# Kernel optimization log

Hardware: AMD Instinct MI355X
Metric: run time of the kernel (lower is better)

The kernel has to match this reference:

```python
import jax, jax.numpy as jnp
import numpy as np

N_LAYERS = 4
D_MODEL = 768
EXPAND = 2
D_INNER = EXPAND * D_MODEL  # 1536
D_STATE = 16
D_CONV = 4
DT_RANK = (D_MODEL + 15) // 16  # 48
BATCH = 2
SEQLEN = 1024


def setup_inputs() -> dict:
    key = jax.random.key(0)
    ks = jax.random.split(key, 7)
    s = 0.02
    x = jax.random.normal(ks[0], (BATCH, SEQLEN, D_MODEL), jnp.float32)
    in_proj_w = jax.random.normal(ks[1], (N_LAYERS, 2 * D_INNER, D_MODEL), jnp.float32) * s
    conv_w = jax.random.normal(ks[2], (N_LAYERS, D_INNER, D_CONV), jnp.float32) * 0.1
    conv_b = jnp.zeros((N_LAYERS, D_INNER), jnp.float32)
    x_proj_w = jax.random.normal(ks[3], (N_LAYERS, DT_RANK + 2 * D_STATE, D_INNER), jnp.float32) * s
    dt_proj_w = jax.random.normal(ks[4], (N_LAYERS, D_INNER, DT_RANK), jnp.float32) * s
    dt_proj_b = jnp.full((N_LAYERS, D_INNER), -4.6, jnp.float32)  # softplus(-4.6) ~= 0.01
    A_log = jnp.broadcast_to(
        jnp.log(jnp.arange(1, D_STATE + 1, dtype=jnp.float32)), (N_LAYERS, D_INNER, D_STATE)
    ) + jnp.zeros((N_LAYERS, D_INNER, D_STATE), jnp.float32)
    D_param = jnp.ones((N_LAYERS, D_INNER), jnp.float32)
    out_proj_w = jax.random.normal(ks[5], (N_LAYERS, D_MODEL, D_INNER), jnp.float32) * s
    return {
        'x': x, 'in_proj_w': in_proj_w, 'conv_w': conv_w, 'conv_b': conv_b,
        'x_proj_w': x_proj_w, 'dt_proj_w': dt_proj_w, 'dt_proj_b': dt_proj_b,
        'A_log': A_log, 'D_param': D_param, 'out_proj_w': out_proj_w,
    }


def _mamba_block(x, ipw, cw, cb, xpw, dpw, dpb, alog, dparam, opw):
    Bsz = x.shape[0]
    # input projection -> gate z and ssm stream u
    xz = jnp.einsum('bld,ed->ble', x, ipw)          # [B,L,2*d_inner]
    u, z = jnp.split(xz, 2, axis=-1)
    # causal depthwise conv over time + silu
    uc = jnp.swapaxes(u, 1, 2)                      # [B,d_inner,L]
    uc = jax.lax.conv_general_dilated(
        uc, cw[:, None, :], (1,), [(D_CONV - 1, 0)],
        feature_group_count=D_INNER, dimension_numbers=('NCH', 'OIH', 'NCH'))
    u = jax.nn.silu(jnp.swapaxes(uc, 1, 2) + cb)    # [B,L,d_inner]
    # input-dependent SSM parameters
    x_dbl = jnp.einsum('bld,ed->ble', u, xpw)       # [B,L,dt_rank+2*d_state]
    dt, Bm, C = jnp.split(x_dbl, [DT_RANK, DT_RANK + D_STATE], axis=-1)
    delta = jax.nn.softplus(jnp.einsum('blr,dr->bld', dt, dpw) + dpb)  # [B,L,d_inner]
    A = -jnp.exp(alog)                              # [d_inner,d_state]
    dA = jnp.exp(delta[..., None] * A)              # [B,L,d_inner,d_state]
    dBu = (delta * u)[..., None] * Bm[:, :, None, :]  # [B,L,d_inner,d_state]

    def step(h, inp):
        dA_t, dBu_t, C_t = inp
        h = dA_t * h + dBu_t                        # [B,d_inner,d_state]
        return h, jnp.einsum('bdn,bn->bd', h, C_t)

    h0 = jnp.zeros((Bsz, D_INNER, D_STATE), x.dtype)
    _, ys = jax.lax.scan(
        step, h0,
        (jnp.swapaxes(dA, 0, 1), jnp.swapaxes(dBu, 0, 1), jnp.swapaxes(C, 0, 1)))
    y = jnp.swapaxes(ys, 0, 1) + u * dparam         # [B,L,d_inner]
    y = y * jax.nn.silu(z)
    return jnp.einsum('bld,ed->ble', y, opw)        # [B,L,d_model]


def reference(x, in_proj_w, conv_w, conv_b, x_proj_w, dt_proj_w, dt_proj_b, A_log, D_param, out_proj_w):
    for i in range(N_LAYERS):
        x = _mamba_block(x, in_proj_w[i], conv_w[i], conv_b[i], x_proj_w[i],
                         dt_proj_w[i], dt_proj_b[i], A_log[i], D_param[i], out_proj_w[i])
    return x
```

## Files before the change

kernel.cpp:

```cpp
#include <hip/hip_runtime.h>
#include <math.h>

#define NL 4
#define DMODEL 768
#define DINNER 1536
#define DSTATE 16
#define DCONV 4
#define DTRANK 48
#define BATCH 2
#define SEQLEN 1024
#define MTOK (BATCH*SEQLEN)
#define XDIM 80
#define KPAD 64
#define NPAD 96
#define KS2 16
#define KS4 4
#define NCHUNK 64
#define NCSHIFT 6
#define CLEN 16
#define CHSTRIDE (BATCH*16*DINNER)

typedef __bf16 bf16x8 __attribute__((ext_vector_type(8)));
typedef float f32x4 __attribute__((ext_vector_type(4)));

__device__ __forceinline__ void splitbf(float f, unsigned short& hi, unsigned short& lo) {
    unsigned uh = __float_as_uint(f);
    unsigned rh = uh + (0x7fffu + ((uh >> 16) & 1u));
    unsigned short h = (unsigned short)(rh >> 16);
    float fh = __uint_as_float(((unsigned)h) << 16);
    float r = f - fh;
    unsigned ul = __float_as_uint(r);
    unsigned rl = ul + (0x7fffu + ((ul >> 16) & 1u));
    hi = h;
    lo = (unsigned short)(rl >> 16);
}

__device__ __forceinline__ void splitbf4(float4 v, ushort4& h, ushort4& l) {
    splitbf(v.x, h.x, l.x);
    splitbf(v.y, h.y, l.y);
    splitbf(v.z, h.z, l.z);
    splitbf(v.w, h.w, l.w);
}

__device__ __forceinline__ float bf2f(unsigned short h) {
    return __uint_as_float(((unsigned)h) << 16);
}

__device__ __forceinline__ unsigned short f2bf(float f) {
    unsigned u = __float_as_uint(f);
    unsigned r = u + (0x7fffu + ((u >> 16) & 1u));
    return (unsigned short)(r >> 16);
}

__device__ __forceinline__ void pow16(float p, float* pw) {
    float p2 = p * p, p4 = p2 * p2, p8 = p4 * p4;
    pw[0]  = p;          pw[1]  = p2;         pw[2]  = p2 * p;     pw[3]  = p4;
    pw[4]  = p4 * p;     pw[5]  = p4 * p2;    pw[6]  = p4 * pw[2]; pw[7]  = p8;
    pw[8]  = p8 * p;     pw[9]  = p8 * p2;    pw[10] = p8 * pw[2]; pw[11] = p8 * p4;
    pw[12] = p8 * pw[4]; pw[13] = p8 * pw[5]; pw[14] = p8 * pw[6]; pw[15] = p8 * p8;
}

__device__ __forceinline__ void gload_lds16(const void* g, void* l) {
    __builtin_amdgcn_global_load_lds(
        (const __attribute__((address_space(1))) unsigned*)g,
        (__attribute__((address_space(3))) unsigned*)l, 16, 0, 0);
}

#define N_IPW (2 * DINNER * DMODEL / 4)
#define N_OPW (DMODEL * DINNER / 4)
#define N_XPW (NPAD * DINNER / 4)
#define N_DPW (DINNER * KPAD / 4)
#define N_DTP (MTOK * (KPAD - DTRANK) / 4)
#define N_PREP (N_IPW + N_OPW + N_XPW + N_DPW + N_DTP)
#define N_XSPL (MTOK * DMODEL / 4)

__global__ __launch_bounds__(256) void prep_all(
    const float* __restrict__ ipw, const float* __restrict__ opw,
    const float* __restrict__ xpw, const float* __restrict__ dpw,
    const float* __restrict__ x,
    unsigned short* __restrict__ wih, unsigned short* __restrict__ wil,
    unsigned short* __restrict__ woh, unsigned short* __restrict__ wol,
    unsigned short* __restrict__ wxh,
    unsigned short* __restrict__ wdh,
    unsigned short* __restrict__ dth,
    unsigned short* __restrict__ ah, unsigned short* __restrict__ al)
{
    const int L = blockIdx.y;
    int i = blockIdx.x * 256 + threadIdx.x;
    if (i < N_IPW) {
        float4 v = ((const float4*)(ipw + (size_t)L * 2 * DINNER * DMODEL))[i];
        ushort4 h, l;
        splitbf4(v, h, l);
        size_t o = (size_t)L * N_IPW + i;
        ((ushort4*)wih)[o] = h;
        ((ushort4*)wil)[o] = l;
        return;
    }
    i -= N_IPW;
    if (i < N_OPW) {
        float4 v = ((const float4*)(opw + (size_t)L * DMODEL * DINNER))[i];
        ushort4 h, l;
        splitbf4(v, h, l);
        size_t o = (size_t)L * N_OPW + i;
        ((ushort4*)woh)[o] = h;
        ((ushort4*)wol)[o] = l;
        return;
    }
    i -= N_OPW;
    if (i < N_XPW) {
        int e = i * 4;
        int row = e / DINNER, col = e % DINNER;
        ushort4 h = {0, 0, 0, 0}, l = {0, 0, 0, 0};
        if (row < XDIM) {
            float4 v = *(const float4*)(xpw + (size_t)L * XDIM * DINNER + (size_t)row * DINNER + col);
            splitbf4(v, h, l);
        }
        size_t o = (size_t)L * N_XPW + i;
        ((ushort4*)wxh)[o] = h;
        return;
    }
    i -= N_XPW;
    if (i < N_DPW) {
        int e = i * 4;
        int row = e >> 6, col = e & 63;
        ushort4 h = {0, 0, 0, 0}, l = {0, 0, 0, 0};
        if (col < DTRANK) {
            float4 v = *(const float4*)(dpw + (size_t)L * DINNER * DTRANK + (size_t)row * DTRANK + col);
            splitbf4(v, h, l);
        }
        size_t o = (size_t)L * N_DPW + i;
        ((ushort4*)wdh)[o] = h;
        return;
    }
    i -= N_DPW;
    if (L != 0) return;
    if (i < N_DTP) {
        int e = i * 4;
        int row = e >> 4, col = DTRANK + (e & 15);
        int o = (row * KPAD + col) / 4;
        ushort4 z = {0, 0, 0, 0};
        ((ushort4*)dth)[o] = z;
        return;
    }
    i -= N_DTP;
    if (i < N_XSPL) {
        float4 v = ((const float4*)x)[i];
        ushort4 h, l;
        splitbf4(v, h, l);
        ((ushort4*)ah)[i] = h;
        ((ushort4*)al)[i] = l;
    }
}

template<int BM, int BN, int BK, int EPI, int PREC>
__global__ __launch_bounds__(256, (BM >= 128 ? 2 : 4)) void gemm_pre(
    const unsigned short* __restrict__ Ah, const unsigned short* __restrict__ Al, int lda,
    const unsigned short* __restrict__ Wh, const unsigned short* __restrict__ Wl, int ldw,
    float* __restrict__ C, float* __restrict__ Caux, int ldc, int Klen, size_t zstride, int nclip,
    const float* __restrict__ bias)
{
    constexpr int MT = BM / 32, NT = BN / 32;
    constexpr int WPR = BK / 8;
    constexpr int ACH = BM * WPR;
    constexpr int WCH = BN * WPR;
    __shared__ unsigned short sAh[BM * BK];
    __shared__ unsigned short sWh[BN * BK];
    __shared__ unsigned short sAl[PREC == 0 ? BM * BK : 8];
    __shared__ unsigned short sWl[PREC == 0 ? BN * BK : 8];

    const int tid = threadIdx.x;
    const int m0 = blockIdx.y * BM, n0 = blockIdx.x * BN;
    const int kbase = blockIdx.z * Klen;
    C += (size_t)blockIdx.z * zstride;
    const int lane = tid & 63, wave = tid >> 6;
    const int wr = wave >> 1, wc = wave & 1;
    const int wm0 = wr * (BM / 2), wn0 = wc * (BN / 2);
    const int lrow = lane & 15, lq = lane >> 4;

    const bool use_lo = (PREC == 0) && !(EPI == 1 && n0 >= DINNER);

    f32x4 acc[MT][NT];
    #pragma unroll
    for (int mt = 0; mt < MT; mt++)
        #pragma unroll
        for (int nt = 0; nt < NT; nt++) {
            f32x4 z = {0.f, 0.f, 0.f, 0.f};
            acc[mt][nt] = z;
        }

    for (int k0 = kbase; k0 < kbase + Klen; k0 += BK) {
        #pragma unroll
        for (int i = 0; i < (ACH + 255) / 256; i++) {
            int chunk = i * 256 + tid;
            if (ACH % 256 == 0 || chunk < ACH) {
                int r = chunk / WPR, cp = chunk % WPR;
                int c = (BK == 32) ? (cp ^ ((r >> 1) & 3)) : (cp ^ (r & 7));
                size_t goff = (size_t)(m0 + r) * lda + k0 + c * 8;
                gload_lds16(Ah + goff, &sAh[chunk * 8]);
                if (use_lo) gload_lds16(Al + goff, &sAl[chunk * 8]);
            }
        }
        #pragma unroll
        for (int i = 0; i < (WCH + 255) / 256; i++) {
            int chunk = i * 256 + tid;
            if (WCH % 256 == 0 || chunk < WCH) {
                int r = chunk / WPR, cp = chunk % WPR;
                int c = (BK == 32) ? (cp ^ ((r >> 1) & 3)) : (cp ^ (r & 7));
                size_t goff = (size_t)(n0 + r) * ldw + k0 + c * 8;
                gload_lds16(Wh + goff, &sWh[chunk * 8]);
                if (use_lo) gload_lds16(Wl + goff, &sWl[chunk * 8]);
            }
        }
        __syncthreads();

        #pragma unroll
        for (int kk = 0; kk < BK / 32; kk++) {
            bf16x8 fah[MT], fal[MT], fwh[NT], fwl[NT];
            #pragma unroll
            for (int mt = 0; mt < MT; mt++) {
                int rr = wm0 + mt * 16 + lrow;
                int w = (BK == 32) ? (lq ^ ((rr >> 1) & 3)) : ((kk * 4 + lq) ^ (rr & 7));
                int off = rr * BK + w * 8;
                fah[mt] = *(const bf16x8*)&sAh[off];
                if (use_lo) fal[mt] = *(const bf16x8*)&sAl[off];
            }
            #pragma unroll
            for (int nt = 0; nt < NT; nt++) {
                int rr = wn0 + nt * 16 + lrow;
                int w = (BK == 32) ? (lq ^ ((rr >> 1) & 3)) : ((kk * 4 + lq) ^ (rr & 7));
                int off = rr * BK + w * 8;
                fwh[nt] = *(const bf16x8*)&sWh[off];
                if (use_lo) fwl[nt] = *(const bf16x8*)&sWl[off];
            }
            #pragma unroll
            for (int mt = 0; mt < MT; mt++)
                #pragma unroll
                for (int nt = 0; nt < NT; nt++)
                    acc[mt][nt] = __builtin_amdgcn_mfma_f32_16x16x32_bf16(fah[mt], fwh[nt], acc[mt][nt], 0, 0, 0);
            if (use_lo) {
                #pragma unroll
                for (int mt = 0; mt < MT; mt++)
                    #pragma unroll
                    for (int nt = 0; nt < NT; nt++) {
                        acc[mt][nt] = __builtin_amdgcn_mfma_f32_16x16x32_bf16(fah[mt], fwl[nt], acc[mt][nt], 0, 0, 0);
                        acc[mt][nt] = __builtin_amdgcn_mfma_f32_16x16x32_bf16(fal[mt], fwh[nt], acc[mt][nt], 0, 0, 0);
                    }
            }
        }
        __syncthreads();
    }

    #pragma unroll
    for (int mt = 0; mt < MT; mt++)
        #pragma unroll
        for (int nt = 0; nt < NT; nt++) {
            int row0 = m0 + wm0 + mt * 16 + lq * 4;
            int col  = n0 + wn0 + nt * 16 + lrow;
            if constexpr (EPI == 0) {
                #pragma unroll
                for (int i = 0; i < 4; i++)
                    if (col < nclip) C[(size_t)(row0 + i) * ldc + col] = acc[mt][nt][i];
            } else if constexpr (EPI == 1) {
                if (col < DINNER) {
                    #pragma unroll
                    for (int i = 0; i < 4; i++)
                        C[(size_t)(row0 + i) * DINNER + col] = acc[mt][nt][i];
                } else {
                    #pragma unroll
                    for (int i = 0; i < 4; i++)
                        Caux[(size_t)(row0 + i) * DINNER + (col - DINNER)] = acc[mt][nt][i];
                }
            } else {
                unsigned short* Cb = (unsigned short*)C;
                float bc = bias[col];
                #pragma unroll
                for (int i = 0; i < 4; i++) {
                    float t = acc[mt][nt][i] + bc;
                    float e = __expf(-fabsf(t));
                    float v = fmaxf(t, 0.f) + __logf(1.f + e);
                    Cb[(size_t)(row0 + i) * ldc + col] = f2bf(v);
                }
            }
        }
}

template<int MODE>
__global__ __launch_bounds__(256) void reduce4(
    const float* __restrict__ part, float* __restrict__ dst,
    unsigned short* __restrict__ hi, unsigned short* __restrict__ lo)
{
    constexpr size_t S = (size_t)MTOK * DMODEL / 4;
    int i = blockIdx.x * 256 + threadIdx.x;
    const float4* p = (const float4*)part;
    float4 a = p[i], b = p[i + S], c = p[i + 2 * S], d = p[i + 3 * S];
    float4 s = {a.x + b.x + c.x + d.x, a.y + b.y + c.y + d.y,
                a.z + b.z + c.z + d.z, a.w + b.w + c.w + d.w};
    if (MODE == 0) {
        ((float4*)dst)[i] = s;
    } else {
        ushort4 h, l;
        splitbf4(s, h, l);
        ((ushort4*)hi)[i] = h;
        ((ushort4*)lo)[i] = l;
    }
}

__global__ __launch_bounds__(256) void reduce16(
    const float* __restrict__ part, float* __restrict__ xdbl,
    unsigned short* __restrict__ dth)
{
    constexpr int N4 = MTOK * XDIM / 4;
    constexpr int S4 = MTOK * XDIM / 4;
    int i = blockIdx.x * 256 + threadIdx.x;
    if (i >= N4) return;
    const float4* p = (const float4*)part;
    float4 s = {0.f, 0.f, 0.f, 0.f};
    #pragma unroll
    for (int z = 0; z < KS2; z++) {
        float4 v = p[(size_t)z * S4 + i];
        s.x += v.x; s.y += v.y; s.z += v.z; s.w += v.w;
    }
    ((float4*)xdbl)[i] = s;
    int e = i * 4;
    int col = e % XDIM, row = e / XDIM;
    if (col < DTRANK) {
        ushort4 h, l;
        splitbf4(s, h, l);
        int o = (row * KPAD + col) / 4;
        ((ushort4*)dth)[o] = h;
    }
}

__global__ __launch_bounds__(256) void conv_silu_kernel(
    const float* __restrict__ xu, const float* __restrict__ cw,
    const float* __restrict__ cb,
    unsigned short* __restrict__ uh, unsigned* __restrict__ ut)
{
    int idx = blockIdx.x * 256 + threadIdx.x;
    int d = idx % DINNER;
    int rblk = idx / DINNER;
    int b = rblk >> 6;
    int l0 = (rblk & 63) * 16;
    const float* base = xu + ((size_t)b * SEQLEN + l0) * DINNER + d;
    float w0 = cw[d * 4 + 0], w1 = cw[d * 4 + 1], w2 = cw[d * 4 + 2], w3 = cw[d * 4 + 3];
    float bias = cb[d];
    float xv[19];
    #pragma unroll
    for (int j = 0; j < 3; j++)
        xv[j] = (l0 + j >= 3) ? base[(j - 3) * DINNER] : 0.f;
    #pragma unroll
    for (int j = 3; j < 19; j++)
        xv[j] = base[(j - 3) * DINNER];
    #pragma unroll
    for (int i = 0; i < 16; i++) {
        float acc = bias;
        acc = fmaf(w0, xv[i], acc);
        acc = fmaf(w1, xv[i + 1], acc);
        acc = fmaf(w2, xv[i + 2], acc);
        acc = fmaf(w3, xv[i + 3], acc);
        float uv = acc / (1.f + __expf(-acc));
        unsigned short h, lo_;
        splitbf(uv, h, lo_);
        size_t o = ((size_t)b * SEQLEN + l0 + i) * DINNER + d;
        uh[o] = h;
        ut[o] = ((unsigned)h << 16) | (unsigned)lo_;
    }
}

__global__ __launch_bounds__(256, 3) void scan_pass1(
    const unsigned short* __restrict__ delta, const unsigned* __restrict__ ut,
    const float* __restrict__ xdbl,
    unsigned short* __restrict__ qbuf, float* __restrict__ sdlbuf)
{
    int gid = blockIdx.x * 256 + threadIdx.x;
    int d = gid % DINNER;
    int r = gid / DINNER;
    int chunk = r & (NCHUNK - 1);
    int b = r >> NCSHIFT;
    float q[16];
    #pragma unroll
    for (int n = 0; n < 16; n++) q[n] = 0.f;
    float sdl = 0.f;
    size_t rowbase = (size_t)b * SEQLEN * DINNER + d;
    int t0 = chunk * CLEN;
    #pragma unroll 4
    for (int i = 0; i < CLEN; i++) {
        int t = t0 + i;
        size_t o = rowbase + (size_t)t * DINNER;
        float dl = bf2f(delta[o]);
        unsigned upk = ut[o];
        float uu = bf2f((unsigned short)(upk >> 16)) + bf2f((unsigned short)(upk & 0xffffu));
        float du = dl * uu;
        sdl += dl;
        float pw[16];
        pow16(__expf(-dl), pw);
        const float* Bp = xdbl + (size_t)(b * SEQLEN + t) * XDIM + DTRANK;
        float Bf[16];
        *(float4*)&Bf[0]  = *(const float4*)(Bp + 0);
        *(float4*)&Bf[4]  = *(const float4*)(Bp + 4);
        *(float4*)&Bf[8]  = *(const float4*)(Bp + 8);
        *(float4*)&Bf[12] = *(const float4*)(Bp + 12);
        #pragma unroll
        for (int n = 0; n < 16; n++)
            q[n] = fmaf(pw[n], q[n], du * Bf[n]);
    }
    size_t off = (size_t)((chunk * BATCH + b) * 16) * DINNER + d;
    #pragma unroll
    for (int n = 0; n < 16; n++)
        qbuf[off + (size_t)n * DINNER] = f2bf(q[n]);
    sdlbuf[(size_t)(chunk * BATCH + b) * DINNER + d] = sdl;
}

__global__ __launch_bounds__(256) void scan_pass2(
    const unsigned short* __restrict__ qbuf, const float* __restrict__ sdlbuf,
    unsigned short* __restrict__ hinit)
{
    __shared__ float sP[8][32];
    __shared__ float sQ[8][32];
    int g = threadIdx.x & 31;
    int s = threadIdx.x >> 5;
    int t = blockIdx.x * 32 + g;
    int d = t % DINNER;
    int b = t / (16 * DINNER);
    int n = (t / DINNER) & 15;
    float Arow = -(float)(n + 1);
    float q[8], p[8];
    #pragma unroll
    for (int j = 0; j < 8; j++) {
        int c = s * 8 + j;
        q[j] = bf2f(qbuf[(size_t)c * CHSTRIDE + t]);
        float sdl = sdlbuf[(size_t)(c * BATCH + b) * DINNER + d];
        p[j] = __expf(Arow * sdl);
    }
    float h = 0.f, P = 1.f;
    #pragma unroll
    for (int j = 0; j < 8; j++) {
        h = fmaf(p[j], h, q[j]);
        P *= p[j];
    }
    sP[s][g] = P;
    sQ[s][g] = h;
    __syncthreads();
    float h0 = 0.f;
    for (int j = 0; j < s; j++)
        h0 = fmaf(sP[j][g], h0, sQ[j][g]);
    #pragma unroll
    for (int j = 0; j < 8; j++) {
        int c = s * 8 + j;
        hinit[(size_t)c * CHSTRIDE + t] = f2bf(h0);
        h0 = fmaf(p[j], h0, q[j]);
    }
}

__global__ __launch_bounds__(256, 3) void scan_pass3(
    const unsigned short* __restrict__ delta, const unsigned* __restrict__ ut,
    const float* __restrict__ xdbl, const float* __restrict__ zs,
    const float* __restrict__ Dp, const unsigned short* __restrict__ hinit,
    unsigned short* __restrict__ yh, unsigned short* __restrict__ yl)
{
    int gid = blockIdx.x * 256 + threadIdx.x;
    int d = gid % DINNER;
    int r = gid / DINNER;
    int chunk = r & (NCHUNK - 1);
    int b = r >> NCSHIFT;
    float h[16];
    size_t hoff = (size_t)chunk * CHSTRIDE + (size_t)(b * 16) * DINNER + d;
    #pragma unroll
    for (int n = 0; n < 16; n++) h[n] = bf2f(hinit[hoff + (size_t)n * DINNER]);
    float Dpar = Dp[d];
    size_t rowbase = (size_t)b * SEQLEN * DINNER + d;
    int t0 = chunk * CLEN;
    #pragma unroll 4
    for (int i = 0; i < CLEN; i++) {
        int t = t0 + i;
        size_t o = rowbase + (size_t)t * DINNER;
        float dl = bf2f(delta[o]);
        unsigned upk = ut[o];
        float uu = bf2f((unsigned short)(upk >> 16)) + bf2f((unsigned short)(upk & 0xffffu));
        float du = dl * uu;
        float pw[16];
        pow16(__expf(-dl), pw);
        const float* Bp = xdbl + (size_t)(b * SEQLEN + t) * XDIM + DTRANK;
        float Bf[16], Cf[16];
        *(float4*)&Bf[0]  = *(const float4*)(Bp + 0);
        *(float4*)&Bf[4]  = *(const float4*)(Bp + 4);
        *(float4*)&Bf[8]  = *(const float4*)(Bp + 8);
        *(float4*)&Bf[12] = *(const float4*)(Bp + 12);
        *(float4*)&Cf[0]  = *(const float4*)(Bp + 16);
        *(float4*)&Cf[4]  = *(const float4*)(Bp + 20);
        *(float4*)&Cf[8]  = *(const float4*)(Bp + 24);
        *(float4*)&Cf[12] = *(const float4*)(Bp + 28);
        float yt = 0.f;
        #pragma unroll
        for (int n = 0; n < 16; n++) {
            h[n] = fmaf(pw[n], h[n], du * Bf[n]);
            yt = fmaf(h[n], Cf[n], yt);
        }
        yt = fmaf(uu, Dpar, yt);
        float z = zs[o];
        float sz = z / (1.f + __expf(-z));
        float yv = yt * sz;
        unsigned short hh, ll;
        splitbf(yv, hh, ll);
        yh[o] = hh;
        yl[o] = ll;
    }
}

extern "C" void kernel_launch(void* const* d_in, const int* in_sizes, int n_in,
                              void* d_out, int out_size, void* d_ws, size_t ws_size,
                              hipStream_t stream) {
    const float* x    = (const float*)d_in[0];
    const float* ipw  = (const float*)d_in[1];
    const float* cw   = (const float*)d_in[2];
    const float* cb   = (const float*)d_in[3];
    const float* xpw  = (const float*)d_in[4];
    const float* dpw  = (const float*)d_in[5];
    const float* dpb  = (const float*)d_in[6];
    const float* alog = (const float*)d_in[7];
    const float* dpar = (const float*)d_in[8];
    const float* opw  = (const float*)d_in[9];
    float* out = (float*)d_out;
    (void)alog;

    char* ws = (char*)d_ws;
    float* xu     = (float*)ws;           ws += (size_t)MTOK * DINNER * 4;
    float* zs     = (float*)ws;           ws += (size_t)MTOK * DINNER * 4;
    unsigned short* delta = (unsigned short*)ws; ws += (size_t)MTOK * DINNER * 4;
    float* xdbl   = (float*)ws;           ws += (size_t)MTOK * XDIM * 4;
    unsigned short* qbuf  = (unsigned short*)ws; ws += (size_t)NCHUNK * CHSTRIDE * 4;
    unsigned short* hinit = (unsigned short*)ws; ws += (size_t)NCHUNK * CHSTRIDE * 4;
    float* sdlb   = (float*)ws;           ws += (size_t)NCHUNK * BATCH * DINNER * 4;
    float* part   = (float*)ws;           ws += (size_t)4 * MTOK * DMODEL * 4;
    unsigned short* ah  = (unsigned short*)ws; ws += (size_t)MTOK * DMODEL * 2;
    unsigned short* al  = (unsigned short*)ws; ws += (size_t)MTOK * DMODEL * 2;
    unsigned short* yh  = (unsigned short*)ws; ws += (size_t)MTOK * DINNER * 2;
    unsigned short* yl  = (unsigned short*)ws; ws += (size_t)MTOK * DINNER * 2;
    unsigned short* uh  = (unsigned short*)ws; ws += (size_t)MTOK * DINNER * 2;
    unsigned* ut        = (unsigned*)ws;       ws += (size_t)MTOK * DINNER * 4;
    unsigned short* wih = (unsigned short*)ws; ws += (size_t)NL * 2 * DINNER * DMODEL * 2;
    unsigned short* wil = (unsigned short*)ws; ws += (size_t)NL * 2 * DINNER * DMODEL * 2;
    unsigned short* woh = (unsigned short*)ws; ws += (size_t)NL * DMODEL * DINNER * 2;
    unsigned short* wol = (unsigned short*)ws; ws += (size_t)NL * DMODEL * DINNER * 2;
    unsigned short* wxh = (unsigned short*)ws; ws += (size_t)NL * NPAD * DINNER * 2;
    unsigned short* wdh = (unsigned short*)ws; ws += (size_t)NL * DINNER * KPAD * 2;
    unsigned short* dth = (unsigned short*)ws; ws += (size_t)MTOK * KPAD * 2;

    prep_all<<<dim3((N_PREP + N_XSPL) / 256, NL), 256, 0, stream>>>(
        ipw, opw, xpw, dpw, x,
        wih, wil, woh, wol, wxh, wdh, dth, ah, al);

    for (int L = 0; L < NL; L++) {
        const float* cw_l   = cw   + (size_t)L * DINNER * DCONV;
        const float* cb_l   = cb   + (size_t)L * DINNER;
        const float* dpb_l  = dpb  + (size_t)L * DINNER;
        const float* dpar_l = dpar + (size_t)L * DINNER;
        const unsigned short* wih_l = wih + (size_t)L * 2 * DINNER * DMODEL;
        const unsigned short* wil_l = wil + (size_t)L * 2 * DINNER * DMODEL;
        const unsigned short* woh_l = woh + (size_t)L * DMODEL * DINNER;
        const unsigned short* wol_l = wol + (size_t)L * DMODEL * DINNER;
        const unsigned short* wxh_l = wxh + (size_t)L * NPAD * DINNER;
        const unsigned short* wdh_l = wdh + (size_t)L * DINNER * KPAD;

        gemm_pre<128, 96, 64, 1, 0><<<dim3(2 * DINNER / 96, MTOK / 128, 1), 256, 0, stream>>>(
            ah, al, DMODEL, wih_l, wil_l, DMODEL, xu, zs, DINNER, DMODEL, 0, 1 << 30, nullptr);

        conv_silu_kernel<<<(MTOK / 16) * DINNER / 256, 256, 0, stream>>>(xu, cw_l, cb_l, uh, ut);

        gemm_pre<64, 96, 32, 0, 1><<<dim3(1, MTOK / 64, KS2), 256, 0, stream>>>(
            uh, nullptr, DINNER, wxh_l, nullptr, DINNER, part, nullptr, XDIM,
            DINNER / KS2, (size_t)MTOK * XDIM, XDIM, nullptr);
        reduce16<<<(MTOK * XDIM / 4 + 255) / 256, 256, 0, stream>>>(part, xdbl, dth);

        gemm_pre<128, 96, 64, 2, 1><<<dim3(DINNER / 96, MTOK / 128, 1), 256, 0, stream>>>(
            dth, nullptr, KPAD, wdh_l, nullptr, KPAD, (float*)delta, nullptr, DINNER, KPAD, 0, 1 << 30, dpb_l);

        scan_pass1<<<(BATCH * NCHUNK * DINNER) / 256, 256, 0, stream>>>(
            delta, ut, xdbl, qbuf, sdlb);
        scan_pass2<<<CHSTRIDE * 8 / 256, 256, 0, stream>>>(qbuf, sdlb, hinit);
        scan_pass3<<<(BATCH * NCHUNK * DINNER) / 256, 256, 0, stream>>>(
            delta, ut, xdbl, zs, dpar_l, hinit, yh, yl);

        gemm_pre<128, 96, 64, 0, 0><<<dim3(DMODEL / 96, MTOK / 128, KS4), 256, 0, stream>>>(
            yh, yl, DINNER, woh_l, wol_l, DINNER, part, nullptr, DMODEL,
            DINNER / KS4, (size_t)MTOK * DMODEL, 1 << 30, nullptr);

        int rblocks = MTOK * DMODEL / 4 / 256;
        if (L == NL - 1) {
            reduce4<0><<<rblocks, 256, 0, stream>>>(part, out, nullptr, nullptr);
        } else {
            reduce4<1><<<rblocks, 256, 0, stream>>>(part, nullptr, ah, al);
        }
    }
    (void)in_sizes; (void)n_in; (void)out_size; (void)ws_size;
}
```

Before: 567.4 us.

## Fuse causal conv and SiLU into the x_proj split-K GEMM prologue

Removes the standalone conv_silu kernel and computes the depthwise causal conv plus SiLU inside a new x_proj GEMM kernel. Each block builds its 64x96 bf16 u tile directly in shared memory and writes the packed hi/lo value to ut for the scan. This removes the uh buffer write and re-read along with one kernel launch per layer. The cost is that each block re-reads 4 time-shifted rows of xu, so there is some redundant global traffic, and the stores to ut are now scattered across many small blocks.

After: 641.7 us. 13.1% more time.

```diff
diff --git a/kernel.cpp b/kernel.cpp
--- a/kernel.cpp
+++ b/kernel.cpp
@@ -284,6 +284,99 @@
         }
 }
 
+__global__ __launch_bounds__(256, 4) void gemm2_conv(
+    const float* __restrict__ xu, const float* __restrict__ cw,
+    const float* __restrict__ cb, const unsigned short* __restrict__ Wh,
+    float* __restrict__ part, unsigned* __restrict__ ut)
+{
+    __shared__ unsigned short sU[64 * 112];
+    __shared__ unsigned short sWh[96 * 32];
+    const int tid = threadIdx.x;
+    const int m0 = blockIdx.y * 64;
+    const int kb = blockIdx.z * 96;
+    float* C = part + (size_t)blockIdx.z * ((size_t)MTOK * XDIM);
+
+    #pragma unroll
+    for (int i = 0; i < 24; i++) {
+        int idx = i * 256 + tid;
+        int r = idx / 96, c = idx % 96;
+        int t = m0 + r;
+        int l = t & (SEQLEN - 1);
+        int d = kb + c;
+        const float* bp = xu + (size_t)t * DINNER + d;
+        float w0 = cw[d * 4 + 0], w1 = cw[d * 4 + 1], w2 = cw[d * 4 + 2], w3 = cw[d * 4 + 3];
+        float acc = cb[d];
+        if (l >= 3) acc = fmaf(w0, bp[-3 * DINNER], acc);
+        if (l >= 2) acc = fmaf(w1, bp[-2 * DINNER], acc);
+        if (l >= 1) acc = fmaf(w2, bp[-1 * DINNER], acc);
+        acc = fmaf(w3, bp[0], acc);
+        float uv = acc / (1.f + __expf(-acc));
+        unsigned short h, lo_;
+        splitbf(uv, h, lo_);
+        sU[r * 112 + c] = h;
+        ut[(size_t)t * DINNER + d] = ((unsigned)h << 16) | (unsigned)lo_;
+    }
+
+    const int lane = tid & 63, wave = tid >> 6;
+    const int wr = wave >> 1, wc = wave & 1;
+    const int wm0 = wr * 32, wn0 = wc * 48;
+    const int lrow = lane & 15, lq = lane >> 4;
+
+    f32x4 acc[2][3];
+    #pragma unroll
+    for (int mt = 0; mt < 2; mt++)
+        #pragma unroll
+        for (int nt = 0; nt < 3; nt++) {
+            f32x4 z = {0.f, 0.f, 0.f, 0.f};
+            acc[mt][nt] = z;
+        }
+
+    #pragma unroll
+    for (int ks = 0; ks < 3; ks++) {
+        #pragma unroll
+        for (int i = 0; i < 2; i++) {
+            int chunk = i * 256 + tid;
+            if (chunk < 384) {
+                int r = chunk >> 2, cp = chunk & 3;
+                int c = cp ^ ((r >> 1) & 3);
+                size_t goff = (size_t)r * DINNER + kb + ks * 32 + c * 8;
+                gload_lds16(Wh + goff, &sWh[chunk * 8]);
+            }
+        }
+        __syncthreads();
+
+        bf16x8 fah[2], fwh[3];
+        #pragma unroll
+        for (int mt = 0; mt < 2; mt++) {
+            int rr = wm0 + mt * 16 + lrow;
+            fah[mt] = *(const bf16x8*)&sU[rr * 112 + ks * 32 + lq * 8];
+        }
+        #pragma unroll
+        for (int nt = 0; nt < 3; nt++) {
+            int rr = wn0 + nt * 16 + lrow;
+            int off = rr * 32 + (lq ^ ((rr >> 1) & 3)) * 8;
+            fwh[nt] = *(const bf16x8*)&sWh[off];
+        }
+        #pragma unroll
+        for (int mt = 0; mt < 2; mt++)
+            #pragma unroll
+            for (int nt = 0; nt < 3; nt++)
+                acc[mt][nt] = __builtin_amdgcn_mfma_f32_16x16x32_bf16(fah[mt], fwh[nt], acc[mt][nt], 0, 0, 0);
+        __syncthreads();
+    }
+
+    #pragma unroll
+    for (int mt = 0; mt < 2; mt++)
+        #pragma unroll
+        for (int nt = 0; nt < 3; nt++) {
+            int row0 = m0 + wm0 + mt * 16 + lq * 4;
+            int col  = wn0 + nt * 16 + lrow;
+            #pragma unroll
+            for (int i = 0; i < 4; i++)
+                if (col < XDIM) C[(size_t)(row0 + i) * XDIM + col] = acc[mt][nt][i];
+        }
+}
+
 template<int MODE>
 __global__ __launch_bounds__(256) void reduce4(
     const float* __restrict__ part, float* __restrict__ dst,
@@ -328,42 +421,6 @@
         splitbf4(s, h, l);
         int o = (row * KPAD + col) / 4;
         ((ushort4*)dth)[o] = h;
-    }
-}
-
-__global__ __launch_bounds__(256) void conv_silu_kernel(
-    const float* __restrict__ xu, const float* __restrict__ cw,
-    const float* __restrict__ cb,
-    unsigned short* __restrict__ uh, unsigned* __restrict__ ut)
-{
-    int idx = blockIdx.x * 256 + threadIdx.x;
-    int d = idx % DINNER;
-    int rblk = idx / DINNER;
-    int b = rblk >> 6;
-    int l0 = (rblk & 63) * 16;
-    const float* base = xu + ((size_t)b * SEQLEN + l0) * DINNER + d;
-    float w0 = cw[d * 4 + 0], w1 = cw[d * 4 + 1], w2 = cw[d * 4 + 2], w3 = cw[d * 4 + 3];
-    float bias = cb[d];
-    float xv[19];
-    #pragma unroll
-    for (int j = 0; j < 3; j++)
-        xv[j] = (l0 + j >= 3) ? base[(j - 3) * DINNER] : 0.f;
-    #pragma unroll
-    for (int j = 3; j < 19; j++)
-        xv[j] = base[(j - 3) * DINNER];
-    #pragma unroll
-    for (int i = 0; i < 16; i++) {
-        float acc = bias;
-        acc = fmaf(w0, xv[i], acc);
-        acc = fmaf(w1, xv[i + 1], acc);
-        acc = fmaf(w2, xv[i + 2], acc);
-        acc = fmaf(w3, xv[i + 3], acc);
-        float uv = acc / (1.f + __expf(-acc));
-        unsigned short h, lo_;
-        splitbf(uv, h, lo_);
-        size_t o = ((size_t)b * SEQLEN + l0 + i) * DINNER + d;
-        uh[o] = h;
-        ut[o] = ((unsigned)h << 16) | (unsigned)lo_;
     }
 }
 
@@ -536,7 +593,6 @@
     unsigned short* al  = (unsigned short*)ws; ws += (size_t)MTOK * DMODEL * 2;
     unsigned short* yh  = (unsigned short*)ws; ws += (size_t)MTOK * DINNER * 2;
     unsigned short* yl  = (unsigned short*)ws; ws += (size_t)MTOK * DINNER * 2;
-    unsigned short* uh  = (unsigned short*)ws; ws += (size_t)MTOK * DINNER * 2;
     unsigned* ut        = (unsigned*)ws;       ws += (size_t)MTOK * DINNER * 4;
     unsigned short* wih = (unsigned short*)ws; ws += (size_t)NL * 2 * DINNER * DMODEL * 2;
     unsigned short* wil = (unsigned short*)ws; ws += (size_t)NL * 2 * DINNER * DMODEL * 2;
@@ -565,11 +621,8 @@
         gemm_pre<128, 96, 64, 1, 0><<<dim3(2 * DINNER / 96, MTOK / 128, 1), 256, 0, stream>>>(
             ah, al, DMODEL, wih_l, wil_l, DMODEL, xu, zs, DINNER, DMODEL, 0, 1 << 30, nullptr);
 
-        conv_silu_kernel<<<(MTOK / 16) * DINNER / 256, 256, 0, stream>>>(xu, cw_l, cb_l, uh, ut);
-
-        gemm_pre<64, 96, 32, 0, 1><<<dim3(1, MTOK / 64, KS2), 256, 0, stream>>>(
-            uh, nullptr, DINNER, wxh_l, nullptr, DINNER, part, nullptr, XDIM,
-            DINNER / KS2, (size_t)MTOK * XDIM, XDIM, nullptr);
+        gemm2_conv<<<dim3(1, MTOK / 64, KS2), 256, 0, stream>>>(
+            xu, cw_l, cb_l, wxh_l, part, ut);
         reduce16<<<(MTOK * XDIM / 4 + 255) / 256, 256, 0, stream>>>(part, xdbl, dth);
 
         gemm_pre<128, 96, 64, 2, 1><<<dim3(DINNER / 96, MTOK / 128, 1), 256, 0, stream>>>(
```
